# Kernel tuning notes

Hardware: AMD Instinct MI355X
Metric: run time of the kernel (lower is better)

Reference implementation:

```python
import jax, jax.numpy as jnp
import numpy as np

NUM_HEADS = 32
ROPE_BASE = 10000.0


def _rope_tables(seq_len, dim):
    inv_freq = 1.0 / (ROPE_BASE ** (jnp.arange(0, dim, 2, dtype=jnp.float32) / dim))
    t = jnp.arange(seq_len, dtype=jnp.float32)
    freqs = jnp.outer(t, inv_freq)                      # [S, dim/2]
    emb = jnp.concatenate([freqs, freqs], axis=-1)      # [S, dim]
    return jnp.cos(emb), jnp.sin(emb)


def _rotate_half(x):
    x1, x2 = jnp.split(x, 2, axis=-1)
    return jnp.concatenate([-x2, x1], axis=-1)


def setup_inputs() -> dict:
    key = jax.random.key(0)
    ks = jax.random.split(key, 5)
    B, T, C = 1, 4096, 4096
    hidden_states = jax.random.normal(ks[0], (B, T, C), dtype=jnp.float32)
    position_ids = jnp.arange(B * T, dtype=jnp.int64 if jax.config.jax_enable_x64 else jnp.int32).reshape(B, T)
    s = 0.02
    Wq = jax.random.normal(ks[1], (C, C), dtype=jnp.float32) * s
    Wk = jax.random.normal(ks[2], (C, C), dtype=jnp.float32) * s
    Wv = jax.random.normal(ks[3], (C, C), dtype=jnp.float32) * s
    Wo = jax.random.normal(ks[4], (C, C), dtype=jnp.float32) * s
    return {"hidden_states": hidden_states, "position_ids": position_ids,
            "Wq": Wq, "Wk": Wk, "Wv": Wv, "Wo": Wo}


def reference(hidden_states, position_ids, Wq, Wk, Wv, Wo):
    B, T, C = hidden_states.shape
    nh = NUM_HEADS
    hs = C // nh

    # Projections (torch Linear: x @ W.T), split heads -> [B, nh, T, hs]
    q = (hidden_states @ Wq.T).reshape(B, T, nh, hs).transpose(0, 2, 1, 3)
    k = (hidden_states @ Wk.T).reshape(B, T, nh, hs).transpose(0, 2, 1, 3)
    v = (hidden_states @ Wv.T).reshape(B, T, nh, hs).transpose(0, 2, 1, 3)

    # RoPE (prefill: kv_len == T)
    cos, sin = _rope_tables(T, hs)                      # [T, hs]
    cos_b = cos[position_ids][:, None]                  # [B, 1, T, hs]
    sin_b = sin[position_ids][:, None]
    q = q * cos_b + _rotate_half(q) * sin_b
    k = k * cos_b + _rotate_half(k) * sin_b

    # Eager attention with full [B, nh, T, T] scores (faithful to source)
    scale = hs ** -0.5
    attn = jnp.einsum("bhqd,bhkd->bhqk", q, k) * scale
    causal = jnp.tril(jnp.ones((T, T), dtype=bool))     # diagonal = kv_len - T = 0
    attn = jnp.where(causal[None, None], attn, -jnp.inf)
    attn = jax.nn.softmax(attn, axis=-1)
    out = jnp.einsum("bhqk,bhkd->bhqd", attn, v)
    out = out.transpose(0, 2, 1, 3).reshape(B, T, C)
    return out @ Wo.T
```

## Files before the change

### kernel.cpp

```cpp
#include <hip/hip_runtime.h>

typedef __attribute__((ext_vector_type(8))) short short8;
typedef __attribute__((ext_vector_type(4))) short short4v;
typedef __attribute__((ext_vector_type(4))) float f32x4;

#define NH 32
#define HS 128
#define CDIM 4096
#define QBLK 256
#define KVBLK 64
#define NQT 16

__device__ __forceinline__ ushort f2bf(float f) {
  union { float f; unsigned u; } a; a.f = f;
  unsigned u = a.u;
  return (ushort)((u + 0x7FFFu + ((u >> 16) & 1u)) >> 16);
}
__device__ __forceinline__ float bf2f(ushort h) {
  union { unsigned u; float f; } a; a.u = ((unsigned)h) << 16;
  return a.f;
}
__device__ __forceinline__ unsigned cvtpk_bf16(float lo, float hi) {
  unsigned r;
  asm("v_cvt_pk_bf16_f32 %0, %1, %2" : "=v"(r) : "v"(lo), "v"(hi));
  return r;
}

__device__ __forceinline__ void gld16(const void* g, void* l) {
  __builtin_amdgcn_global_load_lds((const __attribute__((address_space(1))) void*)g,
                                   (__attribute__((address_space(3))) void*)l, 16, 0, 0);
}

__device__ __forceinline__ unsigned lds_off(const void* p) {
  return (unsigned)(uintptr_t)(const __attribute__((address_space(3))) void*)p;
}

template<int OFF>
__device__ __forceinline__ short4v ds_tr16(unsigned addr) {
  short4v r;
  asm volatile("ds_read_b64_tr_b16 %0, %1 offset:%c2" : "=v"(r) : "v"(addr), "i"(OFF));
  return r;
}

__global__ __launch_bounds__(256) void cast_bf16_kernel(const float* __restrict__ in,
                                                        ushort* __restrict__ out, int n4) {
  int i = blockIdx.x * 256 + threadIdx.x;
  if (i >= n4) return;
  float4 v = ((const float4*)in)[i];
  ushort4 o;
  o.x = f2bf(v.x); o.y = f2bf(v.y); o.z = f2bf(v.z); o.w = f2bf(v.w);
  ((ushort4*)out)[i] = o;
}

__global__ __launch_bounds__(256) void cast4_kernel(const float* __restrict__ s0,
                                                    const float* __restrict__ s1,
                                                    const float* __restrict__ s2,
                                                    const float* __restrict__ s3,
                                                    ushort* __restrict__ d0,
                                                    ushort* __restrict__ d1,
                                                    ushort* __restrict__ d2,
                                                    ushort* __restrict__ d3,
                                                    int segBlocks) {
  int b = blockIdx.x;
  int seg = b / segBlocks;
  int i = (b - seg * segBlocks) * 256 + threadIdx.x;
  const float* in = (seg == 0) ? s0 : (seg == 1) ? s1 : (seg == 2) ? s2 : s3;
  ushort* out = (seg == 0) ? d0 : (seg == 1) ? d1 : (seg == 2) ? d2 : d3;
  float4 v = ((const float4*)in)[i];
  ushort4 o;
  o.x = f2bf(v.x); o.y = f2bf(v.y); o.z = f2bf(v.z); o.w = f2bf(v.w);
  ((ushort4*)out)[i] = o;
}

#define A00 0
#define A01 16384
#define A10 32768
#define A11 49152
#define B00 65536
#define B01 81920
#define B10 98304
#define B11 114688

#define GEMM_BODY(OUT_STORE)                                                       \
  __shared__ char sm[131072];                                                      \
  const int tid = threadIdx.x;                                                     \
  const int w = tid >> 6, lane = tid & 63, lhi = lane >> 4, llo = lane & 15;       \
  const char* A0p = (const char*)(A + m0 * 4096);                                  \
  const char* A1p = A0p + 1048576;                                                 \
  const char* B0p = (const char*)(Bp + n0 * 4096);                                 \
  const char* B1p = B0p + 1048576;                                                 \
  const int i0 = tid, i1 = tid + 512;                                              \
  const int ri0 = i0 >> 3, ri1 = i1 >> 3;                                          \
  const int cg0 = (i0 & 7) ^ (((ri0 >> 2) & 1) << 1);                              \
  const int cg1 = (i1 & 7) ^ (((ri1 >> 2) & 1) << 1);                              \
  const int off0 = ri0 * 8192 + cg0 * 16;                                          \
  const int off1 = ri1 * 8192 + cg1 * 16;                                          \
  const unsigned sd0 = (unsigned)(w * 1024);                                       \
  const unsigned sd1 = (unsigned)(8192 + w * 1024);                                \
  const int sw = ((llo >> 2) & 1) << 1;                                            \
  const unsigned rd0 = (unsigned)((llo * 8 + ((0 * 4 + lhi) ^ sw)) * 16);          \
  const unsigned rd1 = (unsigned)((llo * 8 + ((1 * 4 + lhi) ^ sw)) * 16);          \
  const int wmg = w >> 2, wng = w & 3;                                             \
  const unsigned aE = wmg ? A01 : A00;                                             \
  const unsigned aO = wmg ? A11 : A10;                                             \
  const unsigned bE = (wng >> 1) ? B01 : B00;                                      \
  const unsigned bO = (wng >> 1) ? B11 : B10;                                      \
  const unsigned bco = (unsigned)((wng & 1) * 8192);                               \
  f32x4 acc[8][4] = {};                                                            \
  short8 a0[4], a1[4], u0[2], u1[2], v0[2], v1[2];                                 \
  STG(B0p, 0, B00); STG(B1p, 0, B01); STG(A0p, 0, A00); STG(A1p, 0, A01);          \
  STG(B0p, 64, B10); STG(B1p, 64, B11); STG(A0p, 64, A10); STG(A1p, 64, A11);      \
  asm volatile("s_waitcnt vmcnt(8)" ::: "memory");                                 \
  __builtin_amdgcn_s_barrier();                                                    \
  __builtin_amdgcn_sched_barrier(0);                                               \
  for (int it = 0; it < 32; ++it) {                                                \
    const int kc = it * 128;                                                       \
    const bool st = (it < 31);                                                     \
    LDA(aE, 0); LDB(u0, u1, bE, 0);                                                \
    BAR1; MM(0, 0, u0, u1); BAR2;                                                  \
    LDB(v0, v1, bE, 1);                                                            \
    BAR1; MM(0, 1, v0, v1); BAR2;                                                  \
    LDA(aE, 1);                                                                    \
    if (st) STG(B0p, kc + 128, B00);                                               \
    BAR1; MM(1, 1, v0, v1); BAR2;                                                  \
    if (st) { STG(B1p, kc + 128, B01); STG(A0p, kc + 128, A00); }                  \
    BAR1; MM(1, 0, u0, u1);                                                        \
    __builtin_amdgcn_s_setprio(0);                                                 \
    if (st) asm volatile("s_waitcnt vmcnt(6)" ::: "memory");                       \
    else    asm volatile("s_waitcnt vmcnt(0)" ::: "memory");                       \
    __builtin_amdgcn_s_barrier();                                                  \
    LDA(aO, 0); LDB(u0, u1, bO, 0);                                                \
    if (st) STG(A1p, kc + 128, A01);                                               \
    BAR1; MM(0, 0, u0, u1); BAR2;                                                  \
    LDB(v0, v1, bO, 1);                                                            \
    BAR1; MM(0, 1, v0, v1); BAR2;                                                  \
    LDA(aO, 1);                                                                    \
    if (st) { STG(B0p, kc + 192, B10); STG(B1p, kc + 192, B11); }                  \
    BAR1; MM(1, 1, v0, v1); BAR2;                                                  \
    if (st) { STG(A0p, kc + 192, A10); STG(A1p, kc + 192, A11); }                  \
    BAR1; MM(1, 0, u0, u1);                                                        \
    __builtin_amdgcn_s_setprio(0);                                                 \
    if (st) asm volatile("s_waitcnt vmcnt(8)" ::: "memory");                       \
    __builtin_amdgcn_s_barrier();                                                  \
  }                                                                                \
  const int wm = wmg * 128, wn = wng * 64;                                         \
  _Pragma("unroll")                                                                \
  for (int m = 0; m < 8; m++) {                                                    \
    _Pragma("unroll")                                                              \
    for (int nf = 0; nf < 4; nf++) {                                               \
      const size_t col = n0 + wn + nf * 16 + llo;                                  \
      _Pragma("unroll")                                                            \
      for (int j = 0; j < 4; j++) {                                                \
        const size_t row = m0 + wm + m * 16 + lhi * 4 + j;                         \
        OUT_STORE;                                                                 \
      }                                                                            \
    }                                                                              \
  }

#define STG(PAN, K0, LB) do { \
    gld16((PAN) + (size_t)(K0) * 2 + off0, sm + (LB) + sd0); \
    gld16((PAN) + (size_t)(K0) * 2 + off1, sm + (LB) + sd1); \
  } while (0)
#define LDA(BASE, MQ) do { _Pragma("unroll") for (int m_ = 0; m_ < 4; m_++) { \
    a0[m_] = *(const short8*)(sm + (BASE) + (MQ) * 8192 + m_ * 2048 + rd0); \
    a1[m_] = *(const short8*)(sm + (BASE) + (MQ) * 8192 + m_ * 2048 + rd1); } } while (0)
#define LDB(R0, R1, BASE, NQ) do { _Pragma("unroll") for (int n_ = 0; n_ < 2; n_++) { \
    R0[n_] = *(const short8*)(sm + (BASE) + bco + (NQ) * 4096 + n_ * 2048 + rd0); \
    R1[n_] = *(const short8*)(sm + (BASE) + bco + (NQ) * 4096 + n_ * 2048 + rd1); } } while (0)
#define MM(MQ, NQ, R0, R1) do { \
    _Pragma("unroll") for (int m_ = 0; m_ < 4; m_++) _Pragma("unroll") for (int n_ = 0; n_ < 2; n_++) \
      acc[(MQ) * 4 + m_][(NQ) * 2 + n_] = __builtin_amdgcn_mfma_f32_16x16x32_bf16(a0[m_], R0[n_], acc[(MQ) * 4 + m_][(NQ) * 2 + n_], 0, 0, 0); \
    _Pragma("unroll") for (int m_ = 0; m_ < 4; m_++) _Pragma("unroll") for (int n_ = 0; n_ < 2; n_++) \
      acc[(MQ) * 4 + m_][(NQ) * 2 + n_] = __builtin_amdgcn_mfma_f32_16x16x32_bf16(a1[m_], R1[n_], acc[(MQ) * 4 + m_][(NQ) * 2 + n_], 0, 0, 0); \
  } while (0)
#define BAR1 do { __builtin_amdgcn_s_barrier(); \
    asm volatile("s_waitcnt lgkmcnt(0)" ::: "memory"); \
    __builtin_amdgcn_sched_barrier(0); \
    __builtin_amdgcn_s_setprio(1); } while (0)
#define BAR2 do { __builtin_amdgcn_s_setprio(0); __builtin_amdgcn_s_barrier(); } while (0)

__global__ __launch_bounds__(512, 2) void gemm_qkv(const ushort* __restrict__ A,
                                                   const ushort* __restrict__ Bq,
                                                   const ushort* __restrict__ Bk,
                                                   const ushort* __restrict__ Bv,
                                                   ushort* __restrict__ Cq,
                                                   ushort* __restrict__ Ck,
                                                   ushort* __restrict__ Cv) {
  const int bid = blockIdx.x;
  const int seg = bid >> 8;
  const int lb = bid & 255;
  const int x = (lb & 7) * 32 + (lb >> 3);
  const int mt = x >> 4, ntl = x & 15;
  const ushort* Bp;
  ushort* Cp;
  if (seg == 0)      { Bp = Bq; Cp = Cq; }
  else if (seg == 1) { Bp = Bk; Cp = Ck; }
  else               { Bp = Bv; Cp = Cv; }
  const size_t m0 = (size_t)mt * 256, n0 = (size_t)ntl * 256;
  GEMM_BODY(Cp[row * 4096 + col] = f2bf(acc[m][nf][j]));
}

__global__ __launch_bounds__(512, 2) void gemm256f(const ushort* __restrict__ A,
                                                   const ushort* __restrict__ Bp,
                                                   float* __restrict__ C) {
  const int bid = blockIdx.x;
  const int x = (bid & 7) * 32 + (bid >> 3);
  const int mt = x >> 4, nt = x & 15;
  const size_t m0 = (size_t)mt * 256, n0 = (size_t)nt * 256;
  GEMM_BODY(C[row * 4096 + col] = acc[m][nf][j]);
}

#undef STG
#undef LDA
#undef LDB
#undef MM
#undef BAR1
#undef BAR2

__global__ __launch_bounds__(256) void rope_kernel(ushort* __restrict__ Q,
                                                   ushort* __restrict__ Kb,
                                                   const int* __restrict__ pos_ids,
                                                   int nrows) {
  int gid = blockIdx.x * 256 + threadIdx.x;
  int d = gid & 63;
  int row = gid >> 6;
  if (row >= nrows) return;
  int t = row >> 5;
  int pos = pos_ids[t];
  float inv = expf((float)d * -0.14391156831212788f);
  float ang = (float)pos * inv;
  float s, c;
  sincosf(ang, &s, &c);
  size_t base = (size_t)row * HS;
  {
    float x1 = bf2f(Q[base + d]), x2 = bf2f(Q[base + d + 64]);
    Q[base + d]      = f2bf(x1 * c - x2 * s);
    Q[base + d + 64] = f2bf(x2 * c + x1 * s);
  }
  {
    float x1 = bf2f(Kb[base + d]), x2 = bf2f(Kb[base + d + 64]);
    Kb[base + d]      = f2bf(x1 * c - x2 * s);
    Kb[base + d + 64] = f2bf(x2 * c + x1 * s);
  }
}

__global__ __launch_bounds__(512) void flash_attn(const ushort* __restrict__ Q,
                                                  const ushort* __restrict__ K,
                                                  const ushort* __restrict__ V,
                                                  ushort* __restrict__ O) {
  __shared__ __align__(16) ushort Ks[KVBLK * HS];
  __shared__ __align__(16) ushort Vs[KVBLK * HS];
  __shared__ __align__(16) ushort Ps[8][32 * 72];
  const int tid = threadIdx.x;
  const int w = tid >> 6, l = tid & 63, lhi = l >> 4, llo = l & 15;
  const int qbp = blockIdx.x, h = blockIdx.y;

  const int g = llo >> 2, c = llo & 3;
  const int swz = g | ((lhi & 1) << 2);
  const int c1 = c >> 1;
  const int swL = swz & 1, swH = swz & 6;
  const unsigned trbase = lds_off(Vs) + (unsigned)((lhi * 8 + g) * 256 + ((c1 ^ swL) << 4) + (c & 1) * 8);

  const int srow = tid >> 4, sch = tid & 15;
  const int schK = sch ^ (srow & 7);
  const int schV = sch ^ ((srow & 3) | (((srow >> 3) & 1) << 2));

  char* pwB = (char*)Ps[w];
  const float scale = 0.08838834764831845f;

  short8 kreg[2], vreg[2];

  for (int ph = 0; ph < 2; ph++) {
    const int qt = ph ? (NQT - 1 - qbp) : qbp;
    const int qr0 = qt * QBLK + w * 32;
    const int ntile = 4 * qt + 4;

    short8 aq[2][4];
#pragma unroll
    for (int mf = 0; mf < 2; mf++) {
      const ushort* qp = Q + (size_t)(qr0 + mf * 16 + llo) * CDIM + h * HS + lhi * 8;
#pragma unroll
      for (int ki = 0; ki < 4; ki++) aq[mf][ki] = *(const short8*)(qp + ki * 32);
    }

    f32x4 acc[2][8] = {};
    float mrow[2] = {-1e30f, -1e30f};
    float lrow[2] = {0.f, 0.f};

#pragma unroll
    for (int r = 0; r < 2; r++) {
      const size_t rb = (size_t)(srow + r * 32) * CDIM + h * HS + sch * 8;
      kreg[r] = *(const short8*)(K + rb);
      vreg[r] = *(const short8*)(V + rb);
    }
#pragma unroll
    for (int r = 0; r < 2; r++) {
      const int row = srow + r * 32;
      *(short8*)((char*)Ks + ((row * 16 + schK) << 4)) = kreg[r];
      *(short8*)((char*)Vs + ((row * 16 + schV) << 4)) = vreg[r];
    }
    __syncthreads();

    for (int t = 0; t < ntile; t++) {
      const int kv0 = t * KVBLK;
      if (t + 1 < ntile) {
        const size_t rb = (size_t)(kv0 + KVBLK + srow) * CDIM + h * HS + sch * 8;
#pragma unroll
        for (int r = 0; r < 2; r++) {
          kreg[r] = *(const short8*)(K + rb + (size_t)r * 32 * CDIM);
          vreg[r] = *(const short8*)(V + rb + (size_t)r * 32 * CDIM);
        }
      }
      const bool active = (kv0 <= qr0 + 31);
      if (active) {
        f32x4 s[2][4];
        __builtin_amdgcn_s_setprio(1);
#pragma unroll
        for (int nt = 0; nt < 4; nt++) {
          const int krow = nt * 16 + llo;
          const char* kr = (const char*)Ks + krow * 256;
          short8 kf[4];
#pragma unroll
          for (int ki = 0; ki < 4; ki++)
            kf[ki] = *(const short8*)(kr + (((ki * 4 + lhi) ^ (krow & 7)) << 4));
          f32x4 s0 = {0.f, 0.f, 0.f, 0.f}, s1 = {0.f, 0.f, 0.f, 0.f};
#pragma unroll
          for (int ki = 0; ki < 4; ki++) {
            s0 = __builtin_amdgcn_mfma_f32_16x16x32_bf16(kf[ki], aq[0][ki], s0, 0, 0, 0);
            s1 = __builtin_amdgcn_mfma_f32_16x16x32_bf16(kf[ki], aq[1][ki], s1, 0, 0, 0);
          }
          s[0][nt] = s0; s[1][nt] = s1;
        }
        __builtin_amdgcn_s_setprio(0);

        short4v vl0[8], vh0[8];
#pragma unroll
        for (int on = 0; on < 8; on++) {
          unsigned a = trbase + (unsigned)(((on * 2) ^ swH) << 4);
          vl0[on] = ds_tr16<0>(a);
          vh0[on] = ds_tr16<1024>(a);
        }

        const bool needm = (kv0 + KVBLK - 1 > qr0);
#pragma unroll
        for (int mf = 0; mf < 2; mf++) {
          const int qi = qr0 + mf * 16 + llo;
#pragma unroll
          for (int nt = 0; nt < 4; nt++) {
            const int kvb = kv0 + nt * 16 + lhi * 4;
#pragma unroll
            for (int j = 0; j < 4; j++) {
              float sv = s[mf][nt][j] * scale;
              if (needm && kvb + j > qi) sv = -1e30f;
              s[mf][nt][j] = sv;
            }
          }
        }

#pragma unroll
        for (int mf = 0; mf < 2; mf++) {
          f32x4 mm;
#pragma unroll
          for (int j = 0; j < 4; j++)
            mm[j] = fmaxf(fmaxf(s[mf][0][j], s[mf][1][j]), fmaxf(s[mf][2][j], s[mf][3][j]));
          float pmax = fmaxf(fmaxf(mm[0], mm[1]), fmaxf(mm[2], mm[3]));
          pmax = fmaxf(pmax, __shfl_xor(pmax, 16));
          pmax = fmaxf(pmax, __shfl_xor(pmax, 32));
          if (__any(pmax > mrow[mf] + 8.f)) {
            float mn = fmaxf(mrow[mf], pmax);
            float sc = __expf(mrow[mf] - mn);
            mrow[mf] = mn;
            lrow[mf] *= sc;
#pragma unroll
            for (int on = 0; on < 8; on++)
#pragma unroll
              for (int j = 0; j < 4; j++) acc[mf][on][j] *= sc;
          }
          float rs = 0.f;
#pragma unroll
          for (int nt = 0; nt < 4; nt++) {
            float p0 = __expf(s[mf][nt][0] - mrow[mf]);
            float p1 = __expf(s[mf][nt][1] - mrow[mf]);
            float p2 = __expf(s[mf][nt][2] - mrow[mf]);
            float p3 = __expf(s[mf][nt][3] - mrow[mf]);
            rs += (p0 + p1) + (p2 + p3);
            uint2 pk;
            pk.x = cvtpk_bf16(p0, p1);
            pk.y = cvtpk_bf16(p2, p3);
            *(uint2*)(pwB + (mf * 16 + llo) * 144 + nt * 32 + lhi * 8) = pk;
          }
          rs += __shfl_xor(rs, 16);
          rs += __shfl_xor(rs, 32);
          lrow[mf] += rs;
        }

        {
          short8 pf0 = *(const short8*)(pwB + llo * 144 + lhi * 16);
          short8 pf1 = *(const short8*)(pwB + (16 + llo) * 144 + lhi * 16);
          asm volatile("s_waitcnt lgkmcnt(0)" ::: "memory");
          __builtin_amdgcn_sched_barrier(0);
          __builtin_amdgcn_s_setprio(1);
#pragma unroll
          for (int on = 0; on < 8; on++) {
            short8 vf = __builtin_shufflevector(vl0[on], vh0[on], 0, 1, 2, 3, 4, 5, 6, 7);
            acc[0][on] = __builtin_amdgcn_mfma_f32_16x16x32_bf16(vf, pf0, acc[0][on], 0, 0, 0);
            acc[1][on] = __builtin_amdgcn_mfma_f32_16x16x32_bf16(vf, pf1, acc[1][on], 0, 0, 0);
          }
          __builtin_amdgcn_s_setprio(0);
        }
        {
          short8 pf0 = *(const short8*)(pwB + llo * 144 + 64 + lhi * 16);
          short8 pf1 = *(const short8*)(pwB + (16 + llo) * 144 + 64 + lhi * 16);
          short4v vl[8], vh[8];
#pragma unroll
          for (int on = 0; on < 8; on++) {
            unsigned a = trbase + (unsigned)(((on * 2) ^ swH) << 4);
            vl[on] = ds_tr16<8192>(a);
            vh[on] = ds_tr16<9216>(a);
          }
          asm volatile("s_waitcnt lgkmcnt(0)" ::: "memory");
          __builtin_amdgcn_sched_barrier(0);
          __builtin_amdgcn_s_setprio(1);
#pragma unroll
          for (int on = 0; on < 8; on++) {
            short8 vf = __builtin_shufflevector(vl[on], vh[on], 0, 1, 2, 3, 4, 5, 6, 7);
            acc[0][on] = __builtin_amdgcn_mfma_f32_16x16x32_bf16(vf, pf0, acc[0][on], 0, 0, 0);
            acc[1][on] = __builtin_amdgcn_mfma_f32_16x16x32_bf16(vf, pf1, acc[1][on], 0, 0, 0);
          }
          __builtin_amdgcn_s_setprio(0);
        }
      }

      __syncthreads();
      if (t + 1 < ntile) {
#pragma unroll
        for (int r = 0; r < 2; r++) {
          const int row = srow + r * 32;
          *(short8*)((char*)Ks + ((row * 16 + schK) << 4)) = kreg[r];
          *(short8*)((char*)Vs + ((row * 16 + schV) << 4)) = vreg[r];
        }
      }
      __syncthreads();
    }

#pragma unroll
    for (int mf = 0; mf < 2; mf++) {
      const float ri = 1.0f / lrow[mf];
      ushort* orow = O + (size_t)(qr0 + mf * 16 + llo) * CDIM + h * HS + lhi * 4;
#pragma unroll
      for (int on = 0; on < 8; on++) {
        ushort4 o4;
        o4.x = f2bf(acc[mf][on][0] * ri);
        o4.y = f2bf(acc[mf][on][1] * ri);
        o4.z = f2bf(acc[mf][on][2] * ri);
        o4.w = f2bf(acc[mf][on][3] * ri);
        *(ushort4*)(orow + on * 16) = o4;
      }
    }
  }
}

extern "C" void kernel_launch(void* const* d_in, const int* in_sizes, int n_in,
                              void* d_out, int out_size, void* d_ws, size_t ws_size,
                              hipStream_t stream) {
  const float* hs = (const float*)d_in[0];
  const int* pos = (const int*)d_in[1];
  const float* Wq = (const float*)d_in[2];
  const float* Wk = (const float*)d_in[3];
  const float* Wv = (const float*)d_in[4];
  const float* Wo = (const float*)d_in[5];
  float* out = (float*)d_out;

  const int T = 4096;
  const size_t elems = (size_t)T * CDIM;

  ushort* hsb  = (ushort*)d_ws;
  ushort* wbuf = hsb + elems;
  ushort* qb   = wbuf + elems;
  ushort* kb   = qb + elems;
  ushort* vb   = kb + elems;

  ushort* wkb = (ushort*)d_out;
  ushort* wvb = wkb + elems;

  const int n4 = (int)(elems / 4);
  const int castBlocks = (n4 + 255) / 256;

  cast4_kernel<<<castBlocks * 4, 256, 0, stream>>>(hs, Wq, Wk, Wv, hsb, wbuf, wkb, wvb, castBlocks);

  gemm_qkv<<<768, 512, 0, stream>>>(hsb, wbuf, wkb, wvb, qb, kb, vb);

  rope_kernel<<<(T * NH * 64) / 256, 256, 0, stream>>>(qb, kb, pos, T * NH);

  flash_attn<<<dim3(NQT / 2, NH), 512, 0, stream>>>(qb, kb, vb, hsb);

  cast_bf16_kernel<<<castBlocks, 256, 0, stream>>>(Wo, wbuf, n4);
  gemm256f<<<256, 512, 0, stream>>>(hsb, wbuf, out);
}
```

Before: 809.4 us.

## Double-buffer K/V tiles in LDS using direct global-to-LDS loads

Doubles the K and V shared-memory tiles and fills the next tile straight from global memory into LDS with direct-to-LDS loads, instead of staging through registers and writing after a barrier. The per-lane mapping is rebuilt so each wave writes a contiguous 1 KB chunk while keeping the existing XOR swizzle. This drops one barrier per KV tile and frees the staging registers, so the prefetch overlaps the current tile's MFMA work. In exchange, LDS use grows substantially, and correctness depends on the load completing before the single remaining barrier.

After: 804.5 us. About the same (-0.6%).

```diff
diff --git a/kernel.cpp b/kernel.cpp
--- a/kernel.cpp
+++ b/kernel.cpp
@@ -248,8 +248,8 @@
                                                   const ushort* __restrict__ K,
                                                   const ushort* __restrict__ V,
                                                   ushort* __restrict__ O) {
-  __shared__ __align__(16) ushort Ks[KVBLK * HS];
-  __shared__ __align__(16) ushort Vs[KVBLK * HS];
+  __shared__ __align__(16) ushort Ks[2][KVBLK * HS];
+  __shared__ __align__(16) ushort Vs[2][KVBLK * HS];
   __shared__ __align__(16) ushort Ps[8][32 * 72];
   const int tid = threadIdx.x;
   const int w = tid >> 6, l = tid & 63, lhi = l >> 4, llo = l & 15;
@@ -259,16 +259,23 @@
   const int swz = g | ((lhi & 1) << 2);
   const int c1 = c >> 1;
   const int swL = swz & 1, swH = swz & 6;
-  const unsigned trbase = lds_off(Vs) + (unsigned)((lhi * 8 + g) * 256 + ((c1 ^ swL) << 4) + (c & 1) * 8);
-
-  const int srow = tid >> 4, sch = tid & 15;
-  const int schK = sch ^ (srow & 7);
-  const int schV = sch ^ ((srow & 3) | (((srow >> 3) & 1) << 2));
+  const unsigned trconst = (unsigned)((lhi * 8 + g) * 256 + ((c1 ^ swL) << 4) + (c & 1) * 8);
+
+  const int r0 = w * 4 + lhi;
+  const int cgK = llo ^ (r0 & 7);
+  const int cgV = llo ^ ((r0 & 3) | (((r0 >> 3) & 1) << 2));
 
   char* pwB = (char*)Ps[w];
   const float scale = 0.08838834764831845f;
 
-  short8 kreg[2], vreg[2];
+#define STAGE(T1) do { \
+    const ushort* kp_ = K + (size_t)((T1) * KVBLK + r0) * CDIM + h * HS + cgK * 8; \
+    const ushort* vp_ = V + (size_t)((T1) * KVBLK + r0) * CDIM + h * HS + cgV * 8; \
+    char* kd_ = (char*)Ks[(T1) & 1] + w * 1024; \
+    char* vd_ = (char*)Vs[(T1) & 1] + w * 1024; \
+    gld16(kp_, kd_); gld16(kp_ + (size_t)32 * CDIM, kd_ + 8192); \
+    gld16(vp_, vd_); gld16(vp_ + (size_t)32 * CDIM, vd_ + 8192); \
+  } while (0)
 
   for (int ph = 0; ph < 2; ph++) {
     const int qt = ph ? (NQT - 1 - qbp) : qbp;
@@ -287,38 +294,24 @@
     float mrow[2] = {-1e30f, -1e30f};
     float lrow[2] = {0.f, 0.f};
 
-#pragma unroll
-    for (int r = 0; r < 2; r++) {
-      const size_t rb = (size_t)(srow + r * 32) * CDIM + h * HS + sch * 8;
-      kreg[r] = *(const short8*)(K + rb);
-      vreg[r] = *(const short8*)(V + rb);
-    }
-#pragma unroll
-    for (int r = 0; r < 2; r++) {
-      const int row = srow + r * 32;
-      *(short8*)((char*)Ks + ((row * 16 + schK) << 4)) = kreg[r];
-      *(short8*)((char*)Vs + ((row * 16 + schV) << 4)) = vreg[r];
-    }
+    STAGE(0);
     __syncthreads();
 
     for (int t = 0; t < ntile; t++) {
       const int kv0 = t * KVBLK;
-      if (t + 1 < ntile) {
-        const size_t rb = (size_t)(kv0 + KVBLK + srow) * CDIM + h * HS + sch * 8;
-#pragma unroll
-        for (int r = 0; r < 2; r++) {
-          kreg[r] = *(const short8*)(K + rb + (size_t)r * 32 * CDIM);
-          vreg[r] = *(const short8*)(V + rb + (size_t)r * 32 * CDIM);
-        }
-      }
+      if (t + 1 < ntile) STAGE(t + 1);
+
       const bool active = (kv0 <= qr0 + 31);
       if (active) {
+        const char* ksB = (const char*)Ks[t & 1];
+        const unsigned trb = lds_off(Vs[t & 1]) + trconst;
+
         f32x4 s[2][4];
         __builtin_amdgcn_s_setprio(1);
 #pragma unroll
         for (int nt = 0; nt < 4; nt++) {
           const int krow = nt * 16 + llo;
-          const char* kr = (const char*)Ks + krow * 256;
+          const char* kr = ksB + krow * 256;
           short8 kf[4];
 #pragma unroll
           for (int ki = 0; ki < 4; ki++)
@@ -336,7 +329,7 @@
         short4v vl0[8], vh0[8];
 #pragma unroll
         for (int on = 0; on < 8; on++) {
-          unsigned a = trbase + (unsigned)(((on * 2) ^ swH) << 4);
+          unsigned a = trb + (unsigned)(((on * 2) ^ swH) << 4);
           vl0[on] = ds_tr16<0>(a);
           vh0[on] = ds_tr16<1024>(a);
         }
@@ -414,7 +407,7 @@
           short4v vl[8], vh[8];
 #pragma unroll
           for (int on = 0; on < 8; on++) {
-            unsigned a = trbase + (unsigned)(((on * 2) ^ swH) << 4);
+            unsigned a = trb + (unsigned)(((on * 2) ^ swH) << 4);
             vl[on] = ds_tr16<8192>(a);
             vh[on] = ds_tr16<9216>(a);
           }
@@ -431,15 +424,6 @@
         }
       }
 
-      __syncthreads();
-      if (t + 1 < ntile) {
-#pragma unroll
-        for (int r = 0; r < 2; r++) {
-          const int row = srow + r * 32;
-          *(short8*)((char*)Ks + ((row * 16 + schK) << 4)) = kreg[r];
-          *(short8*)((char*)Vs + ((row * 16 + schV) << 4)) = vreg[r];
-        }
-      }
       __syncthreads();
     }
 
@@ -458,6 +442,7 @@
       }
     }
   }
+#undef STAGE
 }
 
 extern "C" void kernel_launch(void* const* d_in, const int* in_sizes, int n_in,
```
